# Optimization experiments

Hardware: AMD Instinct MI355X
Metric: run time of the kernel (lower is better)

Reference implementation:

```python
import jax, jax.numpy as jnp
import numpy as np

DMODEL = 1024
NHEAD = 16
HDIM = DMODEL // NHEAD
CTXLEN = 2048
BATCH = 2


def setup_inputs() -> dict:
    key = jax.random.key(0)
    k_x, k_qkv, k_pw, k_pb = jax.random.split(key, 4)
    x = jax.random.normal(k_x, (BATCH, CTXLEN, DMODEL), dtype=jnp.float32)
    # nn.Linear weights: stored as [out, in]; init scale ~ 1/sqrt(in)
    s = 1.0 / np.sqrt(DMODEL)
    w_qkv = jax.random.uniform(k_qkv, (3 * DMODEL, DMODEL), minval=-s, maxval=s, dtype=jnp.float32)
    w_proj = jax.random.uniform(k_pw, (DMODEL, DMODEL), minval=-s, maxval=s, dtype=jnp.float32)
    b_proj = jax.random.uniform(k_pb, (DMODEL,), minval=-s, maxval=s, dtype=jnp.float32)
    return {"x": x, "w_qkv": w_qkv, "w_proj": w_proj, "b_proj": b_proj}


def reference(x, w_qkv, w_proj, b_proj):
    b, t, c = x.shape
    qkv = jnp.einsum('btc,oc->bto', x, w_qkv)  # [b, t, 3c]
    q, k, v = jnp.split(qkv, 3, axis=-1)
    # [b, nhead, t, hdim]
    q = q.reshape(b, t, NHEAD, HDIM).transpose(0, 2, 1, 3)
    k = k.reshape(b, t, NHEAD, HDIM).transpose(0, 2, 1, 3)
    v = v.reshape(b, t, NHEAD, HDIM).transpose(0, 2, 1, 3)
    # NOTE: original code MULTIPLIES by sqrt(hdim) (not the usual divide)
    att = jnp.einsum('bhqd,bhkd->bhqk', q, k) * (HDIM ** 0.5)
    causal = jnp.tril(jnp.ones((t, t), dtype=bool))  # [t, t]
    att = jnp.where(causal[None, None], att, -jnp.inf)
    att = jax.nn.softmax(att, axis=-1)
    y = jnp.einsum('bhqk,bhkd->bhqd', att, v)
    y = y.transpose(0, 2, 1, 3).reshape(b, t, c)
    return jnp.einsum('btc,oc->bto', y, w_proj) + b_proj
```

## Files before the change

kernel.cpp:

```cpp
#include <hip/hip_runtime.h>
#include <hip/hip_bf16.h>

#define DMODEL 1024
#define NHEAD 16
#define HDIM 64
#define CTXLEN 2048
#define BATCH 2
#define M_TOTAL (BATCH * CTXLEN)

typedef unsigned short ushort_t;
typedef __attribute__((ext_vector_type(8))) _Float16 f16x8;
typedef __attribute__((ext_vector_type(8))) unsigned short u16x8;
typedef __attribute__((ext_vector_type(4))) float f32x4;
typedef __attribute__((ext_vector_type(4))) unsigned short u16x4;

#define SCALE_LOG2 11.5415603271f

__device__ __forceinline__ unsigned short f32_f16(float f) {
    return __builtin_bit_cast(unsigned short, (_Float16)f);
}
__device__ __forceinline__ float f16_f32(unsigned short h) {
    return (float)__builtin_bit_cast(_Float16, h);
}
__device__ __forceinline__ float fast_exp2(float x) {
    return __builtin_amdgcn_exp2f(x);
}
__device__ __forceinline__ f32x4 mfma16f(f16x8 a, f16x8 b, f32x4 c) {
    return __builtin_amdgcn_mfma_f32_16x16x32_f16(a, b, c, 0, 0, 0);
}
__device__ __forceinline__ void gload_lds16(const ushort_t* g, ushort_t* l) {
    __builtin_amdgcn_global_load_lds(
        (const __attribute__((address_space(1))) void*)g,
        (__attribute__((address_space(3))) void*)l, 16, 0, 0);
}
__device__ __forceinline__ int unit_off(int qt) {
    if (qt < 8)  return qt;
    if (qt < 16) return 8 + (qt - 8) * 2;
    if (qt < 24) return 24 + (qt - 16) * 3;
    return 48 + (qt - 24) * 4;
}

__global__ __launch_bounds__(256)
void conv3_f32_f16(const float* __restrict__ a, ushort_t* __restrict__ da, int na4,
                   const float* __restrict__ b, ushort_t* __restrict__ db, int nb4,
                   const float* __restrict__ c, ushort_t* __restrict__ dc, int nc4) {
    const int n = na4 + nb4 + nc4;
    for (int i = blockIdx.x * blockDim.x + threadIdx.x; i < n;
         i += gridDim.x * blockDim.x) {
        const float* s; ushort_t* d; int j = i;
        if (j < na4) { s = a; d = da; }
        else if (j - na4 < nb4) { j -= na4; s = b; d = db; }
        else { j -= na4 + nb4; s = c; d = dc; }
        const float4 v = reinterpret_cast<const float4*>(s)[j];
        u16x4 o;
        o[0] = f32_f16(v.x); o[1] = f32_f16(v.y);
        o[2] = f32_f16(v.z); o[3] = f32_f16(v.w);
        reinterpret_cast<u16x4*>(d)[j] = o;
    }
}

template<int BN, bool QKV_EPI>
__global__ __launch_bounds__(256)
void gemm_f16_nt(const ushort_t* __restrict__ A, const ushort_t* __restrict__ B,
                 const float* __restrict__ bias, float* __restrict__ C,
                 ushort_t* __restrict__ qf, ushort_t* __restrict__ kf,
                 ushort_t* __restrict__ vb,
                 int M, int N, int K) {
    constexpr int NF = BN / 32;
    constexpr int BOFF = 4096;
    __shared__ ushort_t lds[BOFF + BN * 32];

    const int tid  = threadIdx.x;
    const int lane = tid & 63;
    const int wave = tid >> 6;
    const int lc   = lane & 15;
    const int lg   = lane >> 4;
    const int wr   = wave >> 1;
    const int wc   = wave & 1;
    const int row0 = blockIdx.y * 128;
    const int col0 = blockIdx.x * BN;

    const int c0 = tid, c1 = 256 + tid;
    const int r0 = c0 >> 2, l0 = (c0 & 3) ^ ((c0 >> 3) & 3);
    const int r1 = c1 >> 2, l1 = (c1 & 3) ^ ((c1 >> 3) & 3);
    const size_t gaoff0 = (size_t)(row0 + r0) * K + l0 * 8;
    const size_t gaoff1 = (size_t)(row0 + r1) * K + l1 * 8;
    const size_t gboff0 = (size_t)(col0 + r0) * K + l0 * 8;
    const size_t gboff1 = (size_t)(col0 + r1) * K + l1 * 8;
    const int ld0 = c0 * 8, ld1 = c1 * 8;

    int aoff[4], boff[NF];
    #pragma unroll
    for (int m = 0; m < 4; ++m) {
        const int ra = wr * 64 + m * 16 + lc;
        aoff[m] = ra * 32 + ((lg ^ ((ra >> 1) & 3)) * 8);
    }
    #pragma unroll
    for (int n = 0; n < NF; ++n) {
        const int rb = wc * (NF * 16) + n * 16 + lc;
        boff[n] = rb * 32 + ((lg ^ ((rb >> 1) & 3)) * 8);
    }

    f32x4 acc[4][NF];
    const f32x4 zero4 = {0.f, 0.f, 0.f, 0.f};
    #pragma unroll
    for (int m = 0; m < 4; ++m)
        #pragma unroll
        for (int n = 0; n < NF; ++n) acc[m][n] = zero4;

    const int NT = K >> 5;

    auto stage = [&](int kt) {
        const int ko = kt * 32;
        gload_lds16(A + gaoff0 + ko, &lds[ld0]);
        gload_lds16(A + gaoff1 + ko, &lds[ld1]);
        gload_lds16(B + gboff0 + ko, &lds[BOFF + ld0]);
        if (BN == 128) gload_lds16(B + gboff1 + ko, &lds[BOFF + ld1]);
    };

    stage(0);
    for (int kt = 0; kt < NT; ++kt) {
        __syncthreads();
        f16x8 fa[4], fb[NF];
        #pragma unroll
        for (int m = 0; m < 4; ++m)
            fa[m] = *reinterpret_cast<const f16x8*>(&lds[aoff[m]]);
        #pragma unroll
        for (int n = 0; n < NF; ++n)
            fb[n] = *reinterpret_cast<const f16x8*>(&lds[BOFF + boff[n]]);
        __syncthreads();
        if (kt + 1 < NT) stage(kt + 1);
        #pragma unroll
        for (int m = 0; m < 4; ++m)
            #pragma unroll
            for (int n = 0; n < NF; ++n)
                acc[m][n] = mfma16f(fa[m], fb[n], acc[m][n]);
    }

    if (!QKV_EPI) {
        #pragma unroll
        for (int m = 0; m < 4; ++m)
            #pragma unroll
            for (int i = 0; i < 4; ++i) {
                const int r = row0 + wr * 64 + m * 16 + lg * 4 + i;
                #pragma unroll
                for (int n = 0; n < NF; ++n) {
                    const int c = col0 + wc * (NF * 16) + n * 16 + lc;
                    C[(size_t)r * N + c] = acc[m][n][i] + bias[c];
                }
            }
    } else {
        #pragma unroll
        for (int m = 0; m < 4; ++m)
            #pragma unroll
            for (int i = 0; i < 4; ++i) {
                const int r = row0 + wr * 64 + m * 16 + lg * 4 + i;
                const int bb = r >> 11;
                const int t  = r & 2047;
                #pragma unroll
                for (int n = 0; n < NF; ++n) {
                    const int cg  = col0 + wc * (NF * 16) + n * 16 + lc;
                    const int sec = cg >> 10;
                    const int ch  = cg & 1023;
                    const int hh  = ch >> 6;
                    const int d   = ch & 63;
                    const size_t off = (((size_t)(bb * NHEAD + hh)) * CTXLEN + t) * HDIM + d;
                    float v = acc[m][n][i];
                    if (sec == 0) v *= SCALE_LOG2;
                    const unsigned short hv = f32_f16(v);
                    if (sec == 0)      qf[off] = hv;
                    else if (sec == 1) kf[off] = hv;
                    else               vb[off] = hv;
                }
            }
    }
}

__global__ __launch_bounds__(256)
void transpose_v(const ushort_t* __restrict__ vb, ushort_t* __restrict__ vt) {
    __shared__ ushort_t T[64][66];
    const int tt = blockIdx.x;
    const int bh = blockIdx.y;
    const int tid = threadIdx.x;
    const int r  = tid >> 2;
    const int c0 = (tid & 3) * 16;

    const ushort_t* src = vb + ((size_t)bh * CTXLEN + tt * 64) * HDIM;
    #pragma unroll
    for (int half = 0; half < 2; ++half) {
        const u16x8 v = *reinterpret_cast<const u16x8*>(&src[(size_t)r * HDIM + c0 + half * 8]);
        #pragma unroll
        for (int j = 0; j < 8; ++j) T[r][c0 + half * 8 + j] = v[j];
    }
    __syncthreads();
    ushort_t* dst = vt + ((size_t)bh * HDIM + r) * CTXLEN + tt * 64 + c0;
    u16x8 o0, o1;
    #pragma unroll
    for (int j = 0; j < 8; ++j) { o0[j] = T[c0 + j][r]; o1[j] = T[c0 + 8 + j][r]; }
    *reinterpret_cast<u16x8*>(&dst[0]) = o0;
    *reinterpret_cast<u16x8*>(&dst[8]) = o1;
}

__global__ __launch_bounds__(256)
void attn_fwd7(const ushort_t* __restrict__ qf, const ushort_t* __restrict__ kf,
               const ushort_t* __restrict__ vt,
               ushort_t* __restrict__ py, float* __restrict__ pml,
               ushort_t* __restrict__ yb) {
    __shared__ ushort_t KH[2][4096];
    __shared__ ushort_t VT[2][4096];
    __shared__ ushort_t Ps[4][16][64];

    const int id    = blockIdx.x;
    const int bh    = id & 31;
    const int u_off = 79 - (id >> 5);
    int qt, u;
    if (u_off < 8)       { qt = u_off;                          u = 0; }
    else if (u_off < 24) { const int t = u_off - 8;  qt = 8  + (t >> 1); u = t & 1; }
    else if (u_off < 48) { const int t = u_off - 24; const int q3 = t / 3; qt = 16 + q3; u = t - q3 * 3; }
    else                 { const int t = u_off - 48; qt = 24 + (t >> 2); u = t & 3; }
    const int total = qt + 1;
    const int nu    = (qt >> 3) + 1;
    const int base  = total / nu, rem = total % nu;
    const int kb0   = u * base + (u < rem ? u : rem);
    const int len   = base + (u < rem ? 1 : 0);
    const int slot  = bh * 80 + u_off;

    const int tid  = threadIdx.x;
    const int wave = tid >> 6;
    const int lane = tid & 63;
    const int lc   = lane & 15;
    const int lg   = lane >> 4;

    const ushort_t* kfb = kf + (size_t)bh * CTXLEN * HDIM;
    const ushort_t* vtb = vt + (size_t)bh * HDIM * CTXLEN;

    const int cA = tid, cB = 256 + tid;
    const int rA = cA >> 3, sgA = (cA & 7) ^ (rA & 7);
    const int rB = cB >> 3, sgB = (cB & 7) ^ (rB & 7);

    auto stage = [&](int kb, int buf) {
        const size_t koff = (size_t)(kb * 64);
        gload_lds16(kfb + (koff + rA) * HDIM + sgA * 8, &KH[buf][cA * 8]);
        gload_lds16(kfb + (koff + rB) * HDIM + sgB * 8, &KH[buf][cB * 8]);
        gload_lds16(vtb + (size_t)rA * CTXLEN + kb * 64 + sgA * 8, &VT[buf][cA * 8]);
        gload_lds16(vtb + (size_t)rB * CTXLEN + kb * 64 + sgB * 8, &VT[buf][cB * 8]);
    };

    const size_t qrow = (size_t)bh * CTXLEN + qt * 64 + wave * 16 + lc;
    f16x8 qfr[2];
    #pragma unroll
    for (int ds = 0; ds < 2; ++ds)
        qfr[ds] = *reinterpret_cast<const f16x8*>(&qf[qrow * HDIM + ds * 32 + lg * 8]);

    const f32x4 zero4 = {0.f, 0.f, 0.f, 0.f};
    f32x4 yacc[4];
    #pragma unroll
    for (int t = 0; t < 4; ++t) yacc[t] = zero4;
    float m_i = -1e30f, l_i = 0.f;

    stage(kb0, 0);
    __syncthreads();

    int cur = 0;
    for (int s = 0; s < len; ++s) {
        const int kb = kb0 + s;
        if (s + 1 < len) stage(kb + 1, cur ^ 1);

        f16x8 kfr[4][2];
        #pragma unroll
        for (int tc = 0; tc < 4; ++tc) {
            const int rk = tc * 16 + lc;
            #pragma unroll
            for (int ds = 0; ds < 2; ++ds) {
                const int a = rk * 64 + (((ds * 4 + lg) ^ (rk & 7)) * 8);
                kfr[tc][ds] = *reinterpret_cast<const f16x8*>(&KH[cur][a]);
            }
        }
        f16x8 vf[4][2];
        #pragma unroll
        for (int t = 0; t < 4; ++t) {
            const int rv = t * 16 + lc;
            #pragma unroll
            for (int ks = 0; ks < 2; ++ks) {
                const int a = rv * 64 + (((ks * 4 + lg) ^ (rv & 7)) * 8);
                vf[t][ks] = *reinterpret_cast<const f16x8*>(&VT[cur][a]);
            }
        }

        f32x4 sacc[4];
        #pragma unroll
        for (int tc = 0; tc < 4; ++tc) sacc[tc] = zero4;
        __builtin_amdgcn_s_setprio(1);
        #pragma unroll
        for (int tc = 0; tc < 4; ++tc)
            #pragma unroll
            for (int ds = 0; ds < 2; ++ds)
                sacc[tc] = mfma16f(kfr[tc][ds], qfr[ds], sacc[tc]);
        __builtin_amdgcn_s_setprio(0);

        float p[4][4];
        #pragma unroll
        for (int tc = 0; tc < 4; ++tc)
            #pragma unroll
            for (int i = 0; i < 4; ++i)
                p[tc][i] = sacc[tc][i];
        if (kb == qt) {
            const int q_loc = wave * 16 + lc;
            #pragma unroll
            for (int tc = 0; tc < 4; ++tc)
                #pragma unroll
                for (int i = 0; i < 4; ++i)
                    if ((tc * 16 + lg * 4 + i) > q_loc) p[tc][i] = -1e30f;
        }
        float mx = p[0][0];
        #pragma unroll
        for (int tc = 0; tc < 4; ++tc)
            #pragma unroll
            for (int i = 0; i < 4; ++i) mx = fmaxf(mx, p[tc][i]);
        mx = fmaxf(mx, __shfl_xor(mx, 16));
        mx = fmaxf(mx, __shfl_xor(mx, 32));

        if (__all(mx <= m_i + 8.0f)) {
            float psum = 0.f;
            #pragma unroll
            for (int tc = 0; tc < 4; ++tc)
                #pragma unroll
                for (int i = 0; i < 4; ++i) {
                    const float e = fast_exp2(p[tc][i] - m_i);
                    p[tc][i] = e;
                    psum += e;
                }
            psum += __shfl_xor(psum, 16);
            psum += __shfl_xor(psum, 32);
            l_i += psum;
        } else {
            const float mnew = fmaxf(m_i, mx);
            const float corr = fast_exp2(m_i - mnew);
            float psum = 0.f;
            #pragma unroll
            for (int tc = 0; tc < 4; ++tc)
                #pragma unroll
                for (int i = 0; i < 4; ++i) {
                    const float e = fast_exp2(p[tc][i] - mnew);
                    p[tc][i] = e;
                    psum += e;
                }
            psum += __shfl_xor(psum, 16);
            psum += __shfl_xor(psum, 32);
            l_i = l_i * corr + psum;
            m_i = mnew;
            #pragma unroll
            for (int t = 0; t < 4; ++t) yacc[t] *= corr;
        }

        #pragma unroll
        for (int tc = 0; tc < 4; ++tc) {
            const int eb = tc * 16 + lg * 4;
            const int se = ((((eb >> 3) ^ (lc & 7)) << 3) | (eb & 7));
            u16x4 pk;
            #pragma unroll
            for (int i = 0; i < 4; ++i) pk[i] = f32_f16(p[tc][i]);
            *reinterpret_cast<u16x4*>(&Ps[wave][lc][se]) = pk;
        }
        f16x8 pa[2];
        #pragma unroll
        for (int ks = 0; ks < 2; ++ks) {
            const int sl = ((ks * 4 + lg) ^ (lc & 7)) << 3;
            pa[ks] = *reinterpret_cast<const f16x8*>(&Ps[wave][lc][sl]);
        }
        __builtin_amdgcn_s_setprio(1);
        #pragma unroll
        for (int t = 0; t < 4; ++t)
            #pragma unroll
            for (int ks = 0; ks < 2; ++ks)
                yacc[t] = mfma16f(vf[t][ks], pa[ks], yacc[t]);
        __builtin_amdgcn_s_setprio(0);

        __syncthreads();
        cur ^= 1;
    }

    const int row = wave * 16 + lc;
    if (nu == 1) {
        const float inv = 1.0f / l_i;
        const int b = bh >> 4, h = bh & 15;
        ushort_t* dst = yb + (size_t)(b * CTXLEN + qt * 64 + row) * DMODEL + h * HDIM;
        #pragma unroll
        for (int t = 0; t < 4; ++t) {
            u16x4 o;
            #pragma unroll
            for (int i = 0; i < 4; ++i) o[i] = f32_f16(yacc[t][i] * inv);
            *reinterpret_cast<u16x4*>(&dst[t * 16 + lg * 4]) = o;
        }
    } else {
        ushort_t* prow = py + ((size_t)slot * 64 + row) * 64;
        #pragma unroll
        for (int t = 0; t < 4; ++t) {
            u16x4 o;
            #pragma unroll
            for (int i = 0; i < 4; ++i) o[i] = f32_f16(yacc[t][i]);
            *reinterpret_cast<u16x4*>(&prow[t * 16 + lg * 4]) = o;
        }
        if (lg == 0) {
            pml[(size_t)slot * 128 + row]      = m_i;
            pml[(size_t)slot * 128 + 64 + row] = l_i;
        }
    }
}

__global__ __launch_bounds__(256)
void merge_attn(const ushort_t* __restrict__ py, const float* __restrict__ pml,
                ushort_t* __restrict__ yb) {
    const int qt  = 8 + blockIdx.x;
    const int bh  = blockIdx.y;
    const int b   = bh >> 4;
    const int h   = bh & 15;
    const int tid = threadIdx.x;
    const int row = tid >> 2;
    const int d0  = (tid & 3) * 16;

    const int nu    = (qt >> 3) + 1;
    const int sbase = bh * 80 + unit_off(qt);

    float mu[4], lu[4];
    float M = -1e30f;
    #pragma unroll
    for (int u = 0; u < 4; ++u) {
        if (u < nu) {
            mu[u] = pml[(size_t)(sbase + u) * 128 + row];
            lu[u] = pml[(size_t)(sbase + u) * 128 + 64 + row];
            M = fmaxf(M, mu[u]);
        } else { mu[u] = -1e30f; lu[u] = 0.f; }
    }
    float w[4], ltot = 0.f;
    #pragma unroll
    for (int u = 0; u < 4; ++u) {
        w[u] = (u < nu) ? fast_exp2(mu[u] - M) : 0.f;
        ltot += w[u] * lu[u];
    }

    float y[16];
    #pragma unroll
    for (int j = 0; j < 16; ++j) y[j] = 0.f;
    #pragma unroll
    for (int u = 0; u < 4; ++u) {
        if (u < nu) {
            const ushort_t* pr = py + ((size_t)(sbase + u) * 64 + row) * 64 + d0;
            const u16x8 a = *reinterpret_cast<const u16x8*>(&pr[0]);
            const u16x8 c = *reinterpret_cast<const u16x8*>(&pr[8]);
            #pragma unroll
            for (int j = 0; j < 8; ++j) {
                y[j]     += w[u] * f16_f32(a[j]);
                y[8 + j] += w[u] * f16_f32(c[j]);
            }
        }
    }
    const float inv = 1.0f / ltot;
    ushort_t* dst = yb + (size_t)(b * CTXLEN + qt * 64 + row) * DMODEL + h * HDIM + d0;
    u16x8 o0, o1;
    #pragma unroll
    for (int j = 0; j < 8; ++j) {
        o0[j] = f32_f16(y[j] * inv);
        o1[j] = f32_f16(y[8 + j] * inv);
    }
    *reinterpret_cast<u16x8*>(&dst[0]) = o0;
    *reinterpret_cast<u16x8*>(&dst[8]) = o1;
}

extern "C" void kernel_launch(void* const* d_in, const int* in_sizes, int n_in,
                              void* d_out, int out_size, void* d_ws, size_t ws_size,
                              hipStream_t stream) {
    const float* x      = (const float*)d_in[0];
    const float* w_qkv  = (const float*)d_in[1];
    const float* w_proj = (const float*)d_in[2];
    const float* b_proj = (const float*)d_in[3];
    float* out = (float*)d_out;

    char* ws = (char*)d_ws;
    ushort_t* wqf = (ushort_t*)(ws);
    ushort_t* wpf = (ushort_t*)(ws + 6291456);
    ushort_t* xf  = (ushort_t*)(ws + 8388608);
    ushort_t* qf  = (ushort_t*)(ws + 16777216);
    ushort_t* kf  = (ushort_t*)(ws + 25165824);
    ushort_t* vb  = (ushort_t*)(ws + 33554432);
    ushort_t* vt  = (ushort_t*)(ws + 41943040);
    ushort_t* py  = (ushort_t*)(ws + 50331648);
    float*    pml = (float*)   (ws + 71303168);
    ushort_t* yb  = xf;

    const dim3 blk(256);

    conv3_f32_f16<<<dim3(2048), blk, 0, stream>>>(
        x, xf, M_TOTAL * DMODEL / 4,
        w_qkv, wqf, 3 * DMODEL * DMODEL / 4,
        w_proj, wpf, DMODEL * DMODEL / 4);

    gemm_f16_nt<128, true><<<dim3(3 * DMODEL / 128, M_TOTAL / 128), blk, 0, stream>>>(
        xf, wqf, nullptr, nullptr, qf, kf, vb, M_TOTAL, 3 * DMODEL, DMODEL);

    transpose_v<<<dim3(CTXLEN / 64, BATCH * NHEAD), blk, 0, stream>>>(vb, vt);

    attn_fwd7<<<dim3(2560), blk, 0, stream>>>(qf, kf, vt, py, pml, yb);
    merge_attn<<<dim3(24, 32), blk, 0, stream>>>(py, pml, yb);

    gemm_f16_nt<64, false><<<dim3(DMODEL / 64, M_TOTAL / 128), blk, 0, stream>>>(
        yb, wpf, b_proj, out, nullptr, nullptr, nullptr, M_TOTAL, DMODEL, DMODEL);
}
```

Baseline: 118.9 us.

## Double GEMM K-tile to 64 with 8-way swizzle and XCD-aware block remap

Raises the GEMM K step from 32 to 64, so each tile stages twice as much A/B data into LDS and issues twice the MFMAs per barrier pair. The LDS swizzle moves to an 8-segment XOR pattern to match the wider rows. Workgroup IDs are also remapped so consecutive tiles land on the same XCD (chunked by 8), aiming for better L2 reuse. This halves loop iterations and barriers but doubles LDS use and fragment registers, which may lower occupancy, and the remap assumes the workgroup count is divisible by 8.

```diff
diff --git a/kernel.cpp b/kernel.cpp
--- a/kernel.cpp
+++ b/kernel.cpp
@@ -67,8 +67,20 @@
                  ushort_t* __restrict__ vb,
                  int M, int N, int K) {
     constexpr int NF = BN / 32;
-    constexpr int BOFF = 4096;
-    __shared__ ushort_t lds[BOFF + BN * 32];
+    constexpr int BOFF = 8192;
+    constexpr int BCHUNK = BN * 8;
+    __shared__ ushort_t lds[BOFF + BN * 64];
+
+    int bx, by;
+    {
+        const int gx  = gridDim.x;
+        const int nwg = gx * (int)gridDim.y;
+        const int cpx = nwg >> 3;
+        int flat = (int)blockIdx.y * gx + (int)blockIdx.x;
+        flat = (flat & 7) * cpx + (flat >> 3);
+        bx = flat % gx;
+        by = flat / gx;
+    }
 
     const int tid  = threadIdx.x;
     const int lane = tid & 63;
@@ -77,28 +89,23 @@
     const int lg   = lane >> 4;
     const int wr   = wave >> 1;
     const int wc   = wave & 1;
-    const int row0 = blockIdx.y * 128;
-    const int col0 = blockIdx.x * BN;
-
-    const int c0 = tid, c1 = 256 + tid;
-    const int r0 = c0 >> 2, l0 = (c0 & 3) ^ ((c0 >> 3) & 3);
-    const int r1 = c1 >> 2, l1 = (c1 & 3) ^ ((c1 >> 3) & 3);
-    const size_t gaoff0 = (size_t)(row0 + r0) * K + l0 * 8;
-    const size_t gaoff1 = (size_t)(row0 + r1) * K + l1 * 8;
-    const size_t gboff0 = (size_t)(col0 + r0) * K + l0 * 8;
-    const size_t gboff1 = (size_t)(col0 + r1) * K + l1 * 8;
-    const int ld0 = c0 * 8, ld1 = c1 * 8;
-
-    int aoff[4], boff[NF];
+    const int row0 = by * 128;
+    const int col0 = bx * BN;
+
+    int aoff[4][2], boff[NF][2];
     #pragma unroll
     for (int m = 0; m < 4; ++m) {
         const int ra = wr * 64 + m * 16 + lc;
-        aoff[m] = ra * 32 + ((lg ^ ((ra >> 1) & 3)) * 8);
+        #pragma unroll
+        for (int kk = 0; kk < 2; ++kk)
+            aoff[m][kk] = ra * 64 + (((kk * 4 + lg) ^ (ra & 7)) * 8);
     }
     #pragma unroll
     for (int n = 0; n < NF; ++n) {
         const int rb = wc * (NF * 16) + n * 16 + lc;
-        boff[n] = rb * 32 + ((lg ^ ((rb >> 1) & 3)) * 8);
+        #pragma unroll
+        for (int kk = 0; kk < 2; ++kk)
+            boff[n][kk] = rb * 64 + (((kk * 4 + lg) ^ (rb & 7)) * 8);
     }
 
     f32x4 acc[4][NF];
@@ -108,33 +115,48 @@
         #pragma unroll
         for (int n = 0; n < NF; ++n) acc[m][n] = zero4;
 
-    const int NT = K >> 5;
+    const int NT = K >> 6;
 
     auto stage = [&](int kt) {
-        const int ko = kt * 32;
-        gload_lds16(A + gaoff0 + ko, &lds[ld0]);
-        gload_lds16(A + gaoff1 + ko, &lds[ld1]);
-        gload_lds16(B + gboff0 + ko, &lds[BOFF + ld0]);
-        if (BN == 128) gload_lds16(B + gboff1 + ko, &lds[BOFF + ld1]);
+        const int ko = kt * 64;
+        #pragma unroll
+        for (int i = 0; i < 4; ++i) {
+            const int c  = tid + i * 256;
+            const int r  = c >> 3;
+            const int sg = (c & 7) ^ (r & 7);
+            gload_lds16(A + (size_t)(row0 + r) * K + ko + sg * 8, &lds[c * 8]);
+        }
+        #pragma unroll
+        for (int i = 0; i < BCHUNK / 256; ++i) {
+            const int c  = tid + i * 256;
+            const int r  = c >> 3;
+            const int sg = (c & 7) ^ (r & 7);
+            gload_lds16(B + (size_t)(col0 + r) * K + ko + sg * 8, &lds[BOFF + c * 8]);
+        }
     };
 
     stage(0);
     for (int kt = 0; kt < NT; ++kt) {
         __syncthreads();
-        f16x8 fa[4], fb[NF];
-        #pragma unroll
-        for (int m = 0; m < 4; ++m)
-            fa[m] = *reinterpret_cast<const f16x8*>(&lds[aoff[m]]);
-        #pragma unroll
-        for (int n = 0; n < NF; ++n)
-            fb[n] = *reinterpret_cast<const f16x8*>(&lds[BOFF + boff[n]]);
+        f16x8 fa[2][4], fb[2][NF];
+        #pragma unroll
+        for (int kk = 0; kk < 2; ++kk) {
+            #pragma unroll
+            for (int m = 0; m < 4; ++m)
+                fa[kk][m] = *reinterpret_cast<const f16x8*>(&lds[aoff[m][kk]]);
+            #pragma unroll
+            for (int n = 0; n < NF; ++n)
+                fb[kk][n] = *reinterpret_cast<const f16x8*>(&lds[BOFF + boff[n][kk]]);
+        }
         __syncthreads();
         if (kt + 1 < NT) stage(kt + 1);
         #pragma unroll
-        for (int m = 0; m < 4; ++m)
-            #pragma unroll
-            for (int n = 0; n < NF; ++n)
-                acc[m][n] = mfma16f(fa[m], fb[n], acc[m][n]);
+        for (int kk = 0; kk < 2; ++kk)
+            #pragma unroll
+            for (int m = 0; m < 4; ++m)
+                #pragma unroll
+                for (int n = 0; n < NF; ++n)
+                    acc[m][n] = mfma16f(fa[kk][m], fb[kk][n], acc[m][n]);
     }
 
     if (!QKV_EPI) {
```

After: 108.6 us. 1.1x faster.
